# Optimization experiments

Measured on AMD Instinct MI355X. Metric: run time of the kernel, lower is better.

Reference implementation:

```python
import jax, jax.numpy as jnp
import numpy as np

N, C, H, W = 8, 64, 128, 128
KS = 3


def setup_inputs() -> dict:
    key = jax.random.key(0)
    k1, k2, k3, k4 = jax.random.split(key, 4)
    gr = jax.random.normal(k1, (N, C, H, W), dtype=jnp.float32)
    gt = jax.random.normal(k2, (N, C, H, W), dtype=jnp.float32)
    # Conv2d(in_channel, 9*in_channel, 3, stride=1, pad=1): weight [O, I, kh, kw], bias [O]
    fan_in = C * KS * KS
    bound = 1.0 / np.sqrt(fan_in)
    Wc = jax.random.uniform(k3, (KS * KS * C, C, KS, KS), dtype=jnp.float32, minval=-bound, maxval=bound)
    bc = jax.random.uniform(k4, (KS * KS * C,), dtype=jnp.float32, minval=-bound, maxval=bound)
    return {"gr": gr, "gt": gt, "Wc": Wc, "bc": bc}


def reference(gr, gt, Wc, bc):
    # dynamic_filter = Conv2d(C, 9C, 3, 1, 1)(gt)
    filt = jax.lax.conv_general_dilated(
        gt, Wc, window_strides=(1, 1), padding=((1, 1), (1, 1)),
        dimension_numbers=("NCHW", "OIHW", "NCHW"),
    ) + bc[None, :, None, None]  # [N, 9C, H, W]

    n, c, h, w = gr.shape
    pad = (KS - 1) // 2
    # replicate padding (torch F.pad mode='replicate' == jnp 'edge')
    grp = jnp.pad(gr, ((0, 0), (0, 0), (pad, pad), (pad, pad)), mode="edge")
    # 3x3 patches as 9 shifted views: [N, C, 9, H, W], index order (kh, kw)
    patches = jnp.stack(
        [grp[:, :, i:i + h, j:j + w] for i in range(KS) for j in range(KS)], axis=2
    )
    # torch code's conv output channel layout is (c, kh, kw); its double transpose
    # of both patches and kernels cancels, so pairing is kernel[c, kh, kw] * patch[c, kh, kw]
    k = filt.reshape(n, c, KS * KS, h, w)
    return jnp.sum(patches * k, axis=2)  # [N, C, H, W]
```

## Files before the change

### kernel.cpp

```cpp
#include <hip/hip_runtime.h>
#include <stdint.h>


typedef short bf16x8 __attribute__((ext_vector_type(8)));
typedef float f32x4 __attribute__((ext_vector_type(4)));

#define ROWBLK_B 16640
#define BTAP_B   18432
#define ZERO_OFF 663552
#define GTB_OFF  (ZERO_OFF + ROWBLK_B)

__device__ __forceinline__ uint32_t f2bf(float f) {
  uint32_t x = __float_as_uint(f);
  return (x + 0x7FFFu + ((x >> 16) & 1u)) >> 16;
}

__device__ __forceinline__ void gload_lds16(const void* g, void* l) {
  __builtin_amdgcn_global_load_lds(
      (const __attribute__((address_space(1))) void*)g,
      (__attribute__((address_space(3))) void*)l, 16, 0, 0);
}

__global__ void prep_wc(const float* __restrict__ Wc, uint8_t* __restrict__ ws) {
  int ch = blockIdx.x * 256 + threadIdx.x;
  int tb = ch / 1152;
  int cw = ch - tb * 1152;
  int tap = tb >> 2, octile = tb & 3;
  int row = cw >> 3, sl = cw & 7;
  int slot = sl ^ (row & 7);
  int ic0 = slot * 8;
  int oc = octile * 144 + (row & 15) * 9 + (row >> 4);
  uint32_t p[4];
#pragma unroll
  for (int e = 0; e < 4; ++e) {
    uint32_t lo = f2bf(Wc[(oc * 64 + ic0 + 2 * e) * 9 + tap]);
    uint32_t hi = f2bf(Wc[(oc * 64 + ic0 + 2 * e + 1) * 9 + tap]);
    p[e] = lo | (hi << 16);
  }
  uint4 u; u.x = p[0]; u.y = p[1]; u.z = p[2]; u.w = p[3];
  *(uint4*)(ws + (size_t)tb * BTAP_B + (size_t)cw * 16) = u;
}

__global__ void prep_gt(const float* __restrict__ gt, uint8_t* __restrict__ ws) {
  int b = blockIdx.x;
  if (b == 1024) {
    uint4 z; z.x = z.y = z.z = z.w = 0;
    for (int i = threadIdx.x; i < 1040; i += 256)
      *(uint4*)(ws + ZERO_OFF + (size_t)i * 16) = z;
    return;
  }
  int n = b >> 7, y = b & 127;
  uint8_t* base = ws + GTB_OFF + (size_t)b * ROWBLK_B;
  for (int i = threadIdx.x; i < 1040; i += 256) {
    int r = i >> 3, sl = i & 7;
    int slot = sl ^ (r & 7);
    uint4 u; u.x = u.y = u.z = u.w = 0;
    if (r >= 1 && r <= 128) {
      int w = r - 1, ic0 = slot * 8;
      uint32_t p[4];
#pragma unroll
      for (int e = 0; e < 4; ++e) {
        uint32_t lo = f2bf(gt[((n * 64 + ic0 + 2 * e) * 128 + y) * 128 + w]);
        uint32_t hi = f2bf(gt[((n * 64 + ic0 + 2 * e + 1) * 128 + y) * 128 + w]);
        p[e] = lo | (hi << 16);
      }
      u.x = p[0]; u.y = p[1]; u.z = p[2]; u.w = p[3];
    }
    *(uint4*)(base + (size_t)i * 16) = u;
  }
}

__global__ __launch_bounds__(512, 2) void dfn_mfma(
    const float* __restrict__ gr, const float* __restrict__ bc,
    const uint8_t* __restrict__ ws, float* __restrict__ out) {
  __shared__ uint8_t smem[156928];
  uint8_t* Abuf = smem;
  uint8_t* Bbuf = smem + 83200;
  const int tid = threadIdx.x;
  const int lane = tid & 63;
  const int wv = tid >> 6;
  const int l15 = lane & 15;
  const int l4 = lane >> 4;
  const int bid = blockIdx.x;
  const int octile = (bid >> 3) & 3;
  const int nh = (bid & 7) | ((bid >> 5) << 3);
  const int n = nh >> 5;
  const int h0 = (nh & 31) * 4;

  int bo[2], aoff[3][2];
#pragma unroll
  for (int kk = 0; kk < 2; ++kk) {
    bo[kk] = l15 * 128 + ((kk * 64 + l4 * 16) ^ ((l15 & 7) << 4));
#pragma unroll
    for (int dwp = 0; dwp < 3; ++dwp) {
      int rl = l15 + dwp;
      aoff[dwp][kk] = rl * 128 + ((kk * 64 + l4 * 16) ^ ((rl & 7) << 4));
    }
  }
  int mrow[4], mcol[4];
#pragma unroll
  for (int mf = 0; mf < 4; ++mf) {
    mrow[mf] = (wv * 4 + mf) >> 3;
    mcol[mf] = ((wv * 4 + mf) & 7) * 2048;
  }

  const uint8_t* gtb = ws + GTB_OFF;
  const uint8_t* zblk = ws + ZERO_OFF;

#define ISSUE_B(T, BUFI) do {                                                 \
    const uint8_t* bsrc_ = ws + (size_t)((T) * 4 + octile) * BTAP_B;          \
    uint8_t* bdst_ = Bbuf + (BUFI) * BTAP_B;                                  \
    _Pragma("unroll")                                                         \
    for (int it = 0; it < 3; ++it) {                                          \
      int idx = it * 512 + tid;                                               \
      if (idx < 1152)                                                         \
        gload_lds16(bsrc_ + (size_t)idx * 16,                                 \
                    bdst_ + (size_t)(it * 512 + (tid & ~63)) * 16);           \
    }                                                                         \
  } while (0)

#define ISSUE_AROW(Y, SLOT) do {                                              \
    int y_ = (Y);                                                             \
    const uint8_t* src_ = (y_ >= 0 && y_ < 128)                               \
        ? (gtb + (size_t)(n * 128 + y_) * ROWBLK_B) : zblk;                   \
    uint8_t* dst_ = Abuf + (SLOT) * ROWBLK_B;                                 \
    _Pragma("unroll")                                                         \
    for (int it = 0; it < 3; ++it) {                                          \
      int idx = it * 512 + tid;                                               \
      if (idx < 1040)                                                         \
        gload_lds16(src_ + (size_t)idx * 16,                                  \
                    dst_ + (size_t)(it * 512 + (tid & ~63)) * 16);            \
    }                                                                         \
  } while (0)

#define TAP(DH, DWP, BUFI) do {                                               \
    const uint8_t* Bcur_ = Bbuf + (BUFI) * BTAP_B;                            \
    _Pragma("unroll")                                                         \
    for (int kk = 0; kk < 2; ++kk) {                                          \
      bf16x8 afr[4];                                                          \
      _Pragma("unroll")                                                       \
      for (int mf = 0; mf < 4; ++mf) {                                        \
        int idx_ = mrow[mf] + ((DH) + 1);                           \
        int slot_ = (idx_ == 5) ? 0 : idx_;     \
        afr[mf] = *(const bf16x8*)(Abuf + slot_ * ROWBLK_B + mcol[mf]         \
                                   + aoff[DWP][kk]);                          \
      }                                                                       \
      const uint8_t* baddr_ = Bcur_ + bo[kk];                                 \
      bf16x8 bq[4];                                                           \
      _Pragma("unroll")                                                       \
      for (int p = 0; p < 4; ++p)                                             \
        bq[p] = *(const bf16x8*)(baddr_ + p * 2048);                          \
      __builtin_amdgcn_s_setprio(1);                                          \
      _Pragma("unroll")                                                       \
      for (int nf = 0; nf < 9; ++nf) {                                        \
        bf16x8 bcur_ = bq[nf & 3];                                            \
        if (nf + 4 < 9)                                                       \
          bq[nf & 3] = *(const bf16x8*)(baddr_ + (nf + 4) * 2048);            \
        _Pragma("unroll")                                                     \
        for (int mf = 0; mf < 4; ++mf)                                        \
          acc[mf][nf] = __builtin_amdgcn_mfma_f32_16x16x32_bf16(              \
              bcur_, afr[mf], acc[mf][nf], 0, 0, 0);                          \
      }                                                                       \
      __builtin_amdgcn_s_setprio(0);                                          \
    }                                                                         \
  } while (0)

#pragma unroll
  for (int row = 0; row < 5; ++row) ISSUE_AROW(h0 - 1 + row, row);
  ISSUE_B(0, 0);
  ISSUE_B(1, 1);

  f32x4 acc[4][9];
#pragma unroll
  for (int nf = 0; nf < 9; ++nf) {
#pragma unroll
    for (int q = 0; q < 4; ++q) {
      float bias = bc[octile * 144 + (l4 * 4 + q) * 9 + nf];
      acc[0][nf][q] = bias; acc[1][nf][q] = bias;
      acc[2][nf][q] = bias; acc[3][nf][q] = bias;
    }
  }
  __syncthreads();

  ISSUE_B(2, 2); ISSUE_B(3, 3);
  TAP(-1, 0, 0); TAP(-1, 1, 1);
  __syncthreads();
  ISSUE_B(4, 0); ISSUE_B(5, 1);
  TAP(-1, 2, 2); TAP(0, 0, 3);
  __syncthreads();
  ISSUE_B(6, 2); ISSUE_B(7, 3);
  ISSUE_AROW(h0 + 4, 0);
  TAP(0, 1, 0); TAP(0, 2, 1);
  __syncthreads();
  ISSUE_B(8, 0);
  TAP(1, 0, 2); TAP(1, 1, 3);
  __syncthreads();
  TAP(1, 2, 0);

  const float* grb = gr + (size_t)(n * 64 + octile * 16 + l4 * 4) * 16384;
  float* outb = out + (size_t)(n * 64 + octile * 16 + l4 * 4) * 16384;
#pragma unroll
  for (int mf = 0; mf < 4; ++mf) {
    int p = (wv * 4 + mf) * 16 + l15;
    int hrow = p >> 7, w = p & 127;
    int h = h0 + hrow;
    int off[3][3];
#pragma unroll
    for (int i = 0; i < 3; ++i) {
      int yy = h + i - 1; yy = yy < 0 ? 0 : (yy > 127 ? 127 : yy);
#pragma unroll
      for (int j = 0; j < 3; ++j) {
        int xx = w + j - 1; xx = xx < 0 ? 0 : (xx > 127 ? 127 : xx);
        off[i][j] = yy * 128 + xx;
      }
    }
#pragma unroll
    for (int q = 0; q < 4; ++q) {
      const float* grc = grb + (size_t)q * 16384;
      float s = 0.f;
#pragma unroll
      for (int i = 0; i < 3; ++i)
#pragma unroll
        for (int j = 0; j < 3; ++j)
          s = fmaf(acc[mf][i * 3 + j][q], grc[off[i][j]], s);
      outb[(size_t)q * 16384 + h * 128 + w] = s;
    }
  }
}

extern "C" void kernel_launch(void* const* d_in, const int* in_sizes, int n_in,
                              void* d_out, int out_size, void* d_ws, size_t ws_size,
                              hipStream_t stream) {
  const float* gr = (const float*)d_in[0];
  const float* gt = (const float*)d_in[1];
  const float* Wc = (const float*)d_in[2];
  const float* bc = (const float*)d_in[3];
  uint8_t* ws = (uint8_t*)d_ws;
  float* out = (float*)d_out;

  prep_wc<<<162, 256, 0, stream>>>(Wc, ws);
  prep_gt<<<1025, 256, 0, stream>>>(gt, ws);
  dfn_mfma<<<1024, 512, 0, stream>>>(gr, bc, ws, out);
}
```

Measured before the change: 96.54 us.

## Load conv weights directly from global into registers, drop LDS B staging

Removes the LDS double-buffering of the weight (B) tiles. Each wave now reads its B fragments straight from global memory into a 6-deep register ring, prefetching across tap boundaries. All six input rows are loaded once up front, so the mid-loop row reload and every intermediate barrier go away. A fragments for the next tap are prefetched during the current tap. LDS use falls from about 157KB to 100KB. In exchange, B reads now depend on global/L2 latency with no shared reuse across waves, which could stall the MFMA pipeline.

After: 103.8 us. +7.5%, slower.

```diff
diff --git a/kernel.cpp b/kernel.cpp
--- a/kernel.cpp
+++ b/kernel.cpp
@@ -73,9 +73,8 @@
 __global__ __launch_bounds__(512, 2) void dfn_mfma(
     const float* __restrict__ gr, const float* __restrict__ bc,
     const uint8_t* __restrict__ ws, float* __restrict__ out) {
-  __shared__ uint8_t smem[156928];
+  __shared__ uint8_t smem[99840];
   uint8_t* Abuf = smem;
-  uint8_t* Bbuf = smem + 83200;
   const int tid = threadIdx.x;
   const int lane = tid & 63;
   const int wv = tid >> 6;
@@ -97,27 +96,15 @@
       aoff[dwp][kk] = rl * 128 + ((kk * 64 + l4 * 16) ^ ((rl & 7) << 4));
     }
   }
-  int mrow[4], mcol[4];
+  int ab[4];
 #pragma unroll
   for (int mf = 0; mf < 4; ++mf) {
-    mrow[mf] = (wv * 4 + mf) >> 3;
-    mcol[mf] = ((wv * 4 + mf) & 7) * 2048;
+    int m = wv * 4 + mf;
+    ab[mf] = (m >> 3) * ROWBLK_B + (m & 7) * 2048;
   }
 
   const uint8_t* gtb = ws + GTB_OFF;
   const uint8_t* zblk = ws + ZERO_OFF;
-
-#define ISSUE_B(T, BUFI) do {                                                 \
-    const uint8_t* bsrc_ = ws + (size_t)((T) * 4 + octile) * BTAP_B;          \
-    uint8_t* bdst_ = Bbuf + (BUFI) * BTAP_B;                                  \
-    _Pragma("unroll")                                                         \
-    for (int it = 0; it < 3; ++it) {                                          \
-      int idx = it * 512 + tid;                                               \
-      if (idx < 1152)                                                         \
-        gload_lds16(bsrc_ + (size_t)idx * 16,                                 \
-                    bdst_ + (size_t)(it * 512 + (tid & ~63)) * 16);           \
-    }                                                                         \
-  } while (0)
 
 #define ISSUE_AROW(Y, SLOT) do {                                              \
     int y_ = (Y);                                                             \
@@ -133,44 +120,52 @@
     }                                                                         \
   } while (0)
 
-#define TAP(DH, DWP, BUFI) do {                                               \
-    const uint8_t* Bcur_ = Bbuf + (BUFI) * BTAP_B;                            \
+  f32x4 acc[4][9];
+  bf16x8 bq[6];
+  bf16x8 afr0[4], afr1[4];
+
+#define TAPX(T, DH, DWP, NDH, NDWP, HASNEXT) do {                             \
     _Pragma("unroll")                                                         \
-    for (int kk = 0; kk < 2; ++kk) {                                          \
-      bf16x8 afr[4];                                                          \
-      _Pragma("unroll")                                                       \
-      for (int mf = 0; mf < 4; ++mf) {                                        \
-        int idx_ = mrow[mf] + ((DH) + 1);                           \
-        int slot_ = (idx_ == 5) ? 0 : idx_;     \
-        afr[mf] = *(const bf16x8*)(Abuf + slot_ * ROWBLK_B + mcol[mf]         \
-                                   + aoff[DWP][kk]);                          \
-      }                                                                       \
-      const uint8_t* baddr_ = Bcur_ + bo[kk];                                 \
-      bf16x8 bq[4];                                                           \
-      _Pragma("unroll")                                                       \
-      for (int p = 0; p < 4; ++p)                                             \
-        bq[p] = *(const bf16x8*)(baddr_ + p * 2048);                          \
+    for (int g = 0; g < 18; ++g) {                                            \
+      const int nf = g % 9;                                                   \
+      bf16x8 bcur_ = bq[g % 6];                                               \
       __builtin_amdgcn_s_setprio(1);                                          \
       _Pragma("unroll")                                                       \
-      for (int nf = 0; nf < 9; ++nf) {                                        \
-        bf16x8 bcur_ = bq[nf & 3];                                            \
-        if (nf + 4 < 9)                                                       \
-          bq[nf & 3] = *(const bf16x8*)(baddr_ + (nf + 4) * 2048);            \
+      for (int mf = 0; mf < 4; ++mf)                                          \
+        acc[mf][nf] = __builtin_amdgcn_mfma_f32_16x16x32_bf16(                \
+            bcur_, (g < 9 ? afr0[mf] : afr1[mf]), acc[mf][nf], 0, 0, 0);      \
+      __builtin_amdgcn_s_setprio(0);                                          \
+      if ((HASNEXT) || g < 12) {                                              \
+        const int f2 = g + 6;                                                 \
+        const int t2 = f2 < 18 ? (T) : (T) + 1;                               \
+        const int ff = f2 < 18 ? f2 : f2 - 18;                                \
+        bq[g % 6] = *(const bf16x8*)(ws + (size_t)(t2 * 4 + octile) * BTAP_B  \
+                                     + bo[ff / 9] + (ff % 9) * 2048);         \
+      }                                                                       \
+      if ((HASNEXT) && g == 8) {                                              \
         _Pragma("unroll")                                                     \
         for (int mf = 0; mf < 4; ++mf)                                        \
-          acc[mf][nf] = __builtin_amdgcn_mfma_f32_16x16x32_bf16(              \
-              bcur_, afr[mf], acc[mf][nf], 0, 0, 0);                          \
+          afr0[mf] = *(const bf16x8*)(Abuf + ab[mf]                           \
+                                      + ((NDH) + 1) * ROWBLK_B               \
+                                      + aoff[NDWP][0]);                       \
       }                                                                       \
-      __builtin_amdgcn_s_setprio(0);                                          \
+      if ((HASNEXT) && g == 17) {                                             \
+        _Pragma("unroll")                                                     \
+        for (int mf = 0; mf < 4; ++mf)                                        \
+          afr1[mf] = *(const bf16x8*)(Abuf + ab[mf]                           \
+                                      + ((NDH) + 1) * ROWBLK_B               \
+                                      + aoff[NDWP][1]);                       \
+      }                                                                       \
     }                                                                         \
   } while (0)
 
 #pragma unroll
-  for (int row = 0; row < 5; ++row) ISSUE_AROW(h0 - 1 + row, row);
-  ISSUE_B(0, 0);
-  ISSUE_B(1, 1);
-
-  f32x4 acc[4][9];
+  for (int row = 0; row < 6; ++row) ISSUE_AROW(h0 - 1 + row, row);
+#pragma unroll
+  for (int f = 0; f < 6; ++f)
+    bq[f] = *(const bf16x8*)(ws + (size_t)octile * BTAP_B
+                             + bo[f / 9] + (f % 9) * 2048);
+
 #pragma unroll
   for (int nf = 0; nf < 9; ++nf) {
 #pragma unroll
@@ -182,20 +177,22 @@
   }
   __syncthreads();
 
-  ISSUE_B(2, 2); ISSUE_B(3, 3);
-  TAP(-1, 0, 0); TAP(-1, 1, 1);
-  __syncthreads();
-  ISSUE_B(4, 0); ISSUE_B(5, 1);
-  TAP(-1, 2, 2); TAP(0, 0, 3);
-  __syncthreads();
-  ISSUE_B(6, 2); ISSUE_B(7, 3);
-  ISSUE_AROW(h0 + 4, 0);
-  TAP(0, 1, 0); TAP(0, 2, 1);
-  __syncthreads();
-  ISSUE_B(8, 0);
-  TAP(1, 0, 2); TAP(1, 1, 3);
-  __syncthreads();
-  TAP(1, 2, 0);
+#pragma unroll
+  for (int mf = 0; mf < 4; ++mf)
+    afr0[mf] = *(const bf16x8*)(Abuf + ab[mf] + aoff[0][0]);
+#pragma unroll
+  for (int mf = 0; mf < 4; ++mf)
+    afr1[mf] = *(const bf16x8*)(Abuf + ab[mf] + aoff[0][1]);
+
+  TAPX(0, -1, 0, -1, 1, 1);
+  TAPX(1, -1, 1, -1, 2, 1);
+  TAPX(2, -1, 2,  0, 0, 1);
+  TAPX(3,  0, 0,  0, 1, 1);
+  TAPX(4,  0, 1,  0, 2, 1);
+  TAPX(5,  0, 2,  1, 0, 1);
+  TAPX(6,  1, 0,  1, 1, 1);
+  TAPX(7,  1, 1,  1, 2, 1);
+  TAPX(8,  1, 2,  0, 0, 0);
 
   const float* grb = gr + (size_t)(n * 64 + octile * 16 + l4 * 4) * 16384;
   float* outb = out + (size_t)(n * 64 + octile * 16 + l4 * 4) * 16384;
```

## Pipeline B-tap loads per tap with partial vmcnt waits instead of full syncs

Applied to the files above, without the earlier changes.

Restructures the load schedule so each wave loads a contiguous chunk of the B tap and A rows, making per-wave vmcnt counts predictable. The paired taps with full __syncthreads are replaced by a one-tap-at-a-time pipeline: each step issues the next B tap, computes the current tap, then waits with a partial s_waitcnt vmcnt(N) and a barrier. This lets loads stay in flight across barriers instead of draining all outstanding loads, at the cost of more barriers and reliance on exact vmcnt accounting for correctness. Buffer reuse distance drops, which raises the risk of reading or overwriting an LDS buffer before its loads finish.

After: 99.93 us. 1.04x slower.

```diff
diff --git a/kernel.cpp b/kernel.cpp
--- a/kernel.cpp
+++ b/kernel.cpp
@@ -110,13 +110,14 @@
 #define ISSUE_B(T, BUFI) do {                                                 \
     const uint8_t* bsrc_ = ws + (size_t)((T) * 4 + octile) * BTAP_B;          \
     uint8_t* bdst_ = Bbuf + (BUFI) * BTAP_B;                                  \
-    _Pragma("unroll")                                                         \
-    for (int it = 0; it < 3; ++it) {                                          \
-      int idx = it * 512 + tid;                                               \
-      if (idx < 1152)                                                         \
-        gload_lds16(bsrc_ + (size_t)idx * 16,                                 \
-                    bdst_ + (size_t)(it * 512 + (tid & ~63)) * 16);           \
-    }                                                                         \
+    const int cb_ = wv * 144;                                                 \
+    gload_lds16(bsrc_ + (size_t)(cb_ + lane) * 16,                            \
+                bdst_ + (size_t)cb_ * 16);                                    \
+    gload_lds16(bsrc_ + (size_t)(cb_ + 64 + lane) * 16,                       \
+                bdst_ + (size_t)(cb_ + 64) * 16);                             \
+    if (lane < 16)                                                            \
+      gload_lds16(bsrc_ + (size_t)(cb_ + 128 + lane) * 16,                    \
+                  bdst_ + (size_t)(cb_ + 128) * 16);                          \
   } while (0)
 
 #define ISSUE_AROW(Y, SLOT) do {                                              \
@@ -124,14 +125,22 @@
     const uint8_t* src_ = (y_ >= 0 && y_ < 128)                               \
         ? (gtb + (size_t)(n * 128 + y_) * ROWBLK_B) : zblk;                   \
     uint8_t* dst_ = Abuf + (SLOT) * ROWBLK_B;                                 \
-    _Pragma("unroll")                                                         \
-    for (int it = 0; it < 3; ++it) {                                          \
-      int idx = it * 512 + tid;                                               \
-      if (idx < 1040)                                                         \
-        gload_lds16(src_ + (size_t)idx * 16,                                  \
-                    dst_ + (size_t)(it * 512 + (tid & ~63)) * 16);            \
-    }                                                                         \
-  } while (0)
+    const int ca_ = wv * 130;                                                 \
+    gload_lds16(src_ + (size_t)(ca_ + lane) * 16,                             \
+                dst_ + (size_t)ca_ * 16);                                     \
+    gload_lds16(src_ + (size_t)(ca_ + 64 + lane) * 16,                        \
+                dst_ + (size_t)(ca_ + 64) * 16);                              \
+    if (lane < 2)                                                             \
+      gload_lds16(src_ + (size_t)(ca_ + 128 + lane) * 16,                     \
+                  dst_ + (size_t)(ca_ + 128) * 16);                           \
+  } while (0)
+
+#define WB(N) do {                                                            \
+    asm volatile("s_waitcnt vmcnt(" #N ")" ::: "memory");                     \
+    __builtin_amdgcn_s_barrier();                                             \
+  } while (0)
+
+  f32x4 acc[4][9];
 
 #define TAP(DH, DWP, BUFI) do {                                               \
     const uint8_t* Bcur_ = Bbuf + (BUFI) * BTAP_B;                            \
@@ -170,7 +179,6 @@
   ISSUE_B(0, 0);
   ISSUE_B(1, 1);
 
-  f32x4 acc[4][9];
 #pragma unroll
   for (int nf = 0; nf < 9; ++nf) {
 #pragma unroll
@@ -180,22 +188,17 @@
       acc[2][nf][q] = bias; acc[3][nf][q] = bias;
     }
   }
-  __syncthreads();
-
-  ISSUE_B(2, 2); ISSUE_B(3, 3);
-  TAP(-1, 0, 0); TAP(-1, 1, 1);
-  __syncthreads();
-  ISSUE_B(4, 0); ISSUE_B(5, 1);
-  TAP(-1, 2, 2); TAP(0, 0, 3);
-  __syncthreads();
-  ISSUE_B(6, 2); ISSUE_B(7, 3);
-  ISSUE_AROW(h0 + 4, 0);
-  TAP(0, 1, 0); TAP(0, 2, 1);
-  __syncthreads();
-  ISSUE_B(8, 0);
-  TAP(1, 0, 2); TAP(1, 1, 3);
-  __syncthreads();
-  TAP(1, 2, 0);
+  WB(3);
+
+  ISSUE_B(2, 2);                      TAP(-1, 0, 0); WB(3);
+  ISSUE_B(3, 3);                      TAP(-1, 1, 1); WB(3);
+  ISSUE_B(4, 0);                      TAP(-1, 2, 2); WB(3);
+  ISSUE_B(5, 1); ISSUE_AROW(h0 + 4, 0); TAP(0, 0, 3); WB(6);
+  ISSUE_B(6, 2);                      TAP(0, 1, 0);  WB(6);
+  ISSUE_B(7, 3);                      TAP(0, 2, 1);  WB(3);
+  ISSUE_B(8, 0);                      TAP(1, 0, 2);  WB(3);
+                                      TAP(1, 1, 3);  WB(0);
+                                      TAP(1, 2, 0);
 
   const float* grb = gr + (size_t)(n * 64 + octile * 16 + l4 * 4) * 16384;
   float* outb = out + (size_t)(n * 64 + octile * 16 + l4 * 4) * 16384;
```

## Load A operand straight from global into registers and stage all B taps in LDS

Applied to the files above, without the earlier changes.

The A (gt image row) fragments no longer go through LDS. Each wave now reads its rows directly from global memory into registers, prefetching the next tap's fragment while the current one is in MFMAs, and the XOR swizzle is dropped from the gt prep layout. This frees LDS, so eight B tap buffers are staged up front and most intermediate barriers go away, leaving only manual vmcnt waits. The risks are that global load latency for A is exposed to the MFMA pipeline, and that the hand-counted vmcnt waits may not match the real number of loads in flight.

Result: slower. 138.6 us (+43.5%).

```diff
diff --git a/kernel.cpp b/kernel.cpp
--- a/kernel.cpp
+++ b/kernel.cpp
@@ -53,10 +53,9 @@
   uint8_t* base = ws + GTB_OFF + (size_t)b * ROWBLK_B;
   for (int i = threadIdx.x; i < 1040; i += 256) {
     int r = i >> 3, sl = i & 7;
-    int slot = sl ^ (r & 7);
     uint4 u; u.x = u.y = u.z = u.w = 0;
     if (r >= 1 && r <= 128) {
-      int w = r - 1, ic0 = slot * 8;
+      int w = r - 1, ic0 = sl * 8;
       uint32_t p[4];
 #pragma unroll
       for (int e = 0; e < 4; ++e) {
@@ -73,9 +72,7 @@
 __global__ __launch_bounds__(512, 2) void dfn_mfma(
     const float* __restrict__ gr, const float* __restrict__ bc,
     const uint8_t* __restrict__ ws, float* __restrict__ out) {
-  __shared__ uint8_t smem[156928];
-  uint8_t* Abuf = smem;
-  uint8_t* Bbuf = smem + 83200;
+  __shared__ uint8_t smem[147456];
   const int tid = threadIdx.x;
   const int lane = tid & 63;
   const int wv = tid >> 6;
@@ -86,30 +83,23 @@
   const int nh = (bid & 7) | ((bid >> 5) << 3);
   const int n = nh >> 5;
   const int h0 = (nh & 31) * 4;
-
-  int bo[2], aoff[3][2];
-#pragma unroll
-  for (int kk = 0; kk < 2; ++kk) {
+  const int arow = wv >> 1;
+
+  int bo[2];
+#pragma unroll
+  for (int kk = 0; kk < 2; ++kk)
     bo[kk] = l15 * 128 + ((kk * 64 + l4 * 16) ^ ((l15 & 7) << 4));
-#pragma unroll
-    for (int dwp = 0; dwp < 3; ++dwp) {
-      int rl = l15 + dwp;
-      aoff[dwp][kk] = rl * 128 + ((kk * 64 + l4 * 16) ^ ((rl & 7) << 4));
-    }
-  }
-  int mrow[4], mcol[4];
-#pragma unroll
-  for (int mf = 0; mf < 4; ++mf) {
-    mrow[mf] = (wv * 4 + mf) >> 3;
-    mcol[mf] = ((wv * 4 + mf) & 7) * 2048;
-  }
+  const int avoff = l15 * 128 + l4 * 16;
+  int mcol[4];
+#pragma unroll
+  for (int mf = 0; mf < 4; ++mf) mcol[mf] = ((wv * 4 + mf) & 7) * 2048;
 
   const uint8_t* gtb = ws + GTB_OFF;
   const uint8_t* zblk = ws + ZERO_OFF;
 
 #define ISSUE_B(T, BUFI) do {                                                 \
     const uint8_t* bsrc_ = ws + (size_t)((T) * 4 + octile) * BTAP_B;          \
-    uint8_t* bdst_ = Bbuf + (BUFI) * BTAP_B;                                  \
+    uint8_t* bdst_ = smem + (size_t)(BUFI) * BTAP_B;                          \
     _Pragma("unroll")                                                         \
     for (int it = 0; it < 3; ++it) {                                          \
       int idx = it * 512 + tid;                                               \
@@ -119,58 +109,50 @@
     }                                                                         \
   } while (0)
 
-#define ISSUE_AROW(Y, SLOT) do {                                              \
-    int y_ = (Y);                                                             \
-    const uint8_t* src_ = (y_ >= 0 && y_ < 128)                               \
-        ? (gtb + (size_t)(n * 128 + y_) * ROWBLK_B) : zblk;                   \
-    uint8_t* dst_ = Abuf + (SLOT) * ROWBLK_B;                                 \
-    _Pragma("unroll")                                                         \
-    for (int it = 0; it < 3; ++it) {                                          \
-      int idx = it * 512 + tid;                                               \
-      if (idx < 1040)                                                         \
-        gload_lds16(src_ + (size_t)idx * 16,                                  \
-                    dst_ + (size_t)(it * 512 + (tid & ~63)) * 16);            \
+#define ISSUE_A(ARR, DH, DWP, KK) do {                                        \
+    int r_ = h0 + arow + (DH);                                                \
+    const uint8_t* ab_ = (r_ >= 0 && r_ < 128)                                \
+        ? (gtb + (size_t)(n * 128 + r_) * ROWBLK_B) : zblk;                   \
+    _Pragma("unroll")                                                         \
+    for (int mf = 0; mf < 4; ++mf)                                            \
+      ARR[mf] = *(const bf16x8*)(ab_ + mcol[mf] + avoff                       \
+                                 + (DWP) * 128 + (KK) * 64);                  \
+  } while (0)
+
+  f32x4 acc[4][9];
+  bf16x8 ar0[4], ar1[4];
+
+#define PHASE(BUFI, KK, ARR) do {                                             \
+    const uint8_t* baddr_ = smem + (size_t)(BUFI) * BTAP_B + bo[KK];          \
+    bf16x8 bq[4];                                                             \
+    _Pragma("unroll")                                                         \
+    for (int p = 0; p < 4; ++p)                                               \
+      bq[p] = *(const bf16x8*)(baddr_ + p * 2048);                            \
+    __builtin_amdgcn_s_setprio(1);                                            \
+    _Pragma("unroll")                                                         \
+    for (int nf = 0; nf < 9; ++nf) {                                          \
+      bf16x8 bcur_ = bq[nf & 3];                                              \
+      if (nf + 4 < 9)                                                         \
+        bq[nf & 3] = *(const bf16x8*)(baddr_ + (nf + 4) * 2048);              \
+      _Pragma("unroll")                                                       \
+      for (int mf = 0; mf < 4; ++mf)                                          \
+        acc[mf][nf] = __builtin_amdgcn_mfma_f32_16x16x32_bf16(                \
+            bcur_, ARR[mf], acc[mf][nf], 0, 0, 0);                            \
     }                                                                         \
-  } while (0)
-
-#define TAP(DH, DWP, BUFI) do {                                               \
-    const uint8_t* Bcur_ = Bbuf + (BUFI) * BTAP_B;                            \
-    _Pragma("unroll")                                                         \
-    for (int kk = 0; kk < 2; ++kk) {                                          \
-      bf16x8 afr[4];                                                          \
-      _Pragma("unroll")                                                       \
-      for (int mf = 0; mf < 4; ++mf) {                                        \
-        int idx_ = mrow[mf] + ((DH) + 1);                           \
-        int slot_ = (idx_ == 5) ? 0 : idx_;     \
-        afr[mf] = *(const bf16x8*)(Abuf + slot_ * ROWBLK_B + mcol[mf]         \
-                                   + aoff[DWP][kk]);                          \
-      }                                                                       \
-      const uint8_t* baddr_ = Bcur_ + bo[kk];                                 \
-      bf16x8 bq[4];                                                           \
-      _Pragma("unroll")                                                       \
-      for (int p = 0; p < 4; ++p)                                             \
-        bq[p] = *(const bf16x8*)(baddr_ + p * 2048);                          \
-      __builtin_amdgcn_s_setprio(1);                                          \
-      _Pragma("unroll")                                                       \
-      for (int nf = 0; nf < 9; ++nf) {                                        \
-        bf16x8 bcur_ = bq[nf & 3];                                            \
-        if (nf + 4 < 9)                                                       \
-          bq[nf & 3] = *(const bf16x8*)(baddr_ + (nf + 4) * 2048);            \
-        _Pragma("unroll")                                                     \
-        for (int mf = 0; mf < 4; ++mf)                                        \
-          acc[mf][nf] = __builtin_amdgcn_mfma_f32_16x16x32_bf16(              \
-              bcur_, afr[mf], acc[mf][nf], 0, 0, 0);                          \
-      }                                                                       \
-      __builtin_amdgcn_s_setprio(0);                                          \
-    }                                                                         \
-  } while (0)
-
-#pragma unroll
-  for (int row = 0; row < 5; ++row) ISSUE_AROW(h0 - 1 + row, row);
-  ISSUE_B(0, 0);
-  ISSUE_B(1, 1);
-
-  f32x4 acc[4][9];
+    __builtin_amdgcn_s_setprio(0);                                            \
+  } while (0)
+
+#define TAP_PF(BUFI, DH, DWP, NDH, NDWP, HASNEXT) do {                        \
+    ISSUE_A(ar1, DH, DWP, 1);                                                 \
+    PHASE(BUFI, 0, ar0);                                                      \
+    if (HASNEXT) ISSUE_A(ar0, NDH, NDWP, 0);                                  \
+    PHASE(BUFI, 1, ar1);                                                      \
+  } while (0)
+
+#pragma unroll
+  for (int t = 0; t < 8; ++t) ISSUE_B(t, t);
+  ISSUE_A(ar0, -1, 0, 0);
+
 #pragma unroll
   for (int nf = 0; nf < 9; ++nf) {
 #pragma unroll
@@ -180,22 +162,24 @@
       acc[2][nf][q] = bias; acc[3][nf][q] = bias;
     }
   }
-  __syncthreads();
-
-  ISSUE_B(2, 2); ISSUE_B(3, 3);
-  TAP(-1, 0, 0); TAP(-1, 1, 1);
-  __syncthreads();
-  ISSUE_B(4, 0); ISSUE_B(5, 1);
-  TAP(-1, 2, 2); TAP(0, 0, 3);
-  __syncthreads();
-  ISSUE_B(6, 2); ISSUE_B(7, 3);
-  ISSUE_AROW(h0 + 4, 0);
-  TAP(0, 1, 0); TAP(0, 2, 1);
-  __syncthreads();
+  asm volatile("s_waitcnt vmcnt(4)" ::: "memory");
+  __builtin_amdgcn_s_barrier();
+
+  TAP_PF(0, -1, 0, -1, 1, 1);
+  __builtin_amdgcn_s_barrier();
   ISSUE_B(8, 0);
-  TAP(1, 0, 2); TAP(1, 1, 3);
-  __syncthreads();
-  TAP(1, 2, 0);
+
+  TAP_PF(1, -1, 1, -1, 2, 1);
+  TAP_PF(2, -1, 2,  0, 0, 1);
+  TAP_PF(3,  0, 0,  0, 1, 1);
+  TAP_PF(4,  0, 1,  0, 2, 1);
+  TAP_PF(5,  0, 2,  1, 0, 1);
+  TAP_PF(6,  1, 0,  1, 1, 1);
+  TAP_PF(7,  1, 1,  1, 2, 1);
+
+  asm volatile("s_waitcnt vmcnt(4)" ::: "memory");
+  __builtin_amdgcn_s_barrier();
+  TAP_PF(0,  1, 2,  0, 0, 0);
 
   const float* grb = gr + (size_t)(n * 64 + octile * 16 + l4 * 4) * 16384;
   float* outb = out + (size_t)(n * 64 + octile * 16 + l4 * 4) * 16384;
```
